# Kernel tuning notes

Hardware: AMD Instinct MI355X
Metric: run time of the kernel (lower is better)

## Reference

```python
import jax, jax.numpy as jnp
import numpy as np

H = 256  # n_hidden


def _lstm_layer(x, W_ih, W_hh, b):
    # x: [B, T, D]; W_ih: [4H, D]; W_hh: [4H, H]; b: [4H]
    B = x.shape[0]
    xg = jnp.einsum('btd,gd->btg', x, W_ih) + b  # [B, T, 4H] input projection, precomputed
    xg = jnp.swapaxes(xg, 0, 1)  # [T, B, 4H] for scan over time

    def step(carry, xt):
        h, c = carry
        g = xt + h @ W_hh.T  # [B, 4H]
        i = jax.nn.sigmoid(g[:, 0 * H:1 * H])
        f = jax.nn.sigmoid(g[:, 1 * H:2 * H])
        gg = jnp.tanh(g[:, 2 * H:3 * H])
        o = jax.nn.sigmoid(g[:, 3 * H:4 * H])
        c = f * c + i * gg
        h = o * jnp.tanh(c)
        return (h, c), h

    init = (jnp.zeros((B, H), x.dtype), jnp.zeros((B, H), x.dtype))
    (_, _), hs = jax.lax.scan(step, init, xg)
    return jnp.swapaxes(hs, 0, 1)  # [B, T, H]


def setup_inputs() -> dict:
    key = jax.random.key(0)
    ks = jax.random.split(key, 9)
    B, T, D, C = 256, 1024, 128, 10
    s_in, s_h = 1.0 / np.sqrt(D), 1.0 / np.sqrt(H)
    return {
        'x': jax.random.normal(ks[0], (B, T, D), jnp.float32),
        'W_ih0': jax.random.normal(ks[1], (4 * H, D), jnp.float32) * s_in,
        'W_hh0': jax.random.normal(ks[2], (4 * H, H), jnp.float32) * s_h,
        'b0': jax.random.normal(ks[3], (4 * H,), jnp.float32) * s_h,
        'W_ih1': jax.random.normal(ks[4], (4 * H, H), jnp.float32) * s_h,
        'W_hh1': jax.random.normal(ks[5], (4 * H, H), jnp.float32) * s_h,
        'b1': jax.random.normal(ks[6], (4 * H,), jnp.float32) * s_h,
        'Wd': jax.random.normal(ks[7], (C, H), jnp.float32) * s_h,
        'bd': jax.random.normal(ks[8], (C,), jnp.float32) * 0.01,
    }


def reference(x, W_ih0, W_hh0, b0, W_ih1, W_hh1, b1, Wd, bd):
    o = _lstm_layer(x, W_ih0, W_hh0, b0)   # layer 1
    o = _lstm_layer(o, W_ih1, W_hh1, b1)   # layer 2
    last = o[:, -1]                         # [B, H] last timestep
    logits = last @ Wd.T + bd               # [B, C]
    return jax.nn.softmax(logits, axis=1)
```

## Files before the change

### kernel.cpp

```cpp
#include <hip/hip_runtime.h>

#define TT 1024

typedef _Float16 f16;
typedef _Float16 f16x8 __attribute__((ext_vector_type(8)));
typedef float f32x4 __attribute__((ext_vector_type(4)));
typedef unsigned long long u64;

__device__ __forceinline__ float sigmoidf_(float x) { return 1.0f / (1.0f + __expf(-x)); }
__device__ __forceinline__ float tanhf_(float x) { return 1.0f - 2.0f / (__expf(2.0f * x) + 1.0f); }

__device__ __forceinline__ f16x8 load_frag_agent(const f16* p) {
  union { u64 v[2]; f16x8 f; } u;
  u.v[0] = __hip_atomic_load((u64*)p,     __ATOMIC_RELAXED, __HIP_MEMORY_SCOPE_AGENT);
  u.v[1] = __hip_atomic_load((u64*)p + 1, __ATOMIC_RELAXED, __HIP_MEMORY_SCOPE_AGENT);
  return u.f;
}

__device__ __forceinline__ void load_h8_sc0(const f16* p, f16x8* a) {
  asm volatile(
      "global_load_dwordx4 %0, %8, off sc0\n\t"
      "global_load_dwordx4 %1, %8, off offset:64 sc0\n\t"
      "global_load_dwordx4 %2, %8, off offset:128 sc0\n\t"
      "global_load_dwordx4 %3, %8, off offset:192 sc0\n\t"
      "global_load_dwordx4 %4, %8, off offset:256 sc0\n\t"
      "global_load_dwordx4 %5, %8, off offset:320 sc0\n\t"
      "global_load_dwordx4 %6, %8, off offset:384 sc0\n\t"
      "global_load_dwordx4 %7, %8, off offset:448 sc0\n\t"
      "s_waitcnt vmcnt(0)"
      : "=&v"(a[0]), "=&v"(a[1]), "=&v"(a[2]), "=&v"(a[3]),
        "=&v"(a[4]), "=&v"(a[5]), "=&v"(a[6]), "=&v"(a[7])
      : "v"(p)
      : "memory");
}
__device__ __forceinline__ void load_h16_sc0(const f16* p0, const f16* p1, f16x8* a) {
  asm volatile(
      "global_load_dwordx4 %0, %16, off sc0\n\t"
      "global_load_dwordx4 %1, %16, off offset:64 sc0\n\t"
      "global_load_dwordx4 %2, %16, off offset:128 sc0\n\t"
      "global_load_dwordx4 %3, %16, off offset:192 sc0\n\t"
      "global_load_dwordx4 %4, %16, off offset:256 sc0\n\t"
      "global_load_dwordx4 %5, %16, off offset:320 sc0\n\t"
      "global_load_dwordx4 %6, %16, off offset:384 sc0\n\t"
      "global_load_dwordx4 %7, %16, off offset:448 sc0\n\t"
      "global_load_dwordx4 %8, %17, off sc0\n\t"
      "global_load_dwordx4 %9, %17, off offset:64 sc0\n\t"
      "global_load_dwordx4 %10, %17, off offset:128 sc0\n\t"
      "global_load_dwordx4 %11, %17, off offset:192 sc0\n\t"
      "global_load_dwordx4 %12, %17, off offset:256 sc0\n\t"
      "global_load_dwordx4 %13, %17, off offset:320 sc0\n\t"
      "global_load_dwordx4 %14, %17, off offset:384 sc0\n\t"
      "global_load_dwordx4 %15, %17, off offset:448 sc0\n\t"
      "s_waitcnt vmcnt(0)"
      : "=&v"(a[0]), "=&v"(a[1]), "=&v"(a[2]), "=&v"(a[3]),
        "=&v"(a[4]), "=&v"(a[5]), "=&v"(a[6]), "=&v"(a[7]),
        "=&v"(a[8]), "=&v"(a[9]), "=&v"(a[10]), "=&v"(a[11]),
        "=&v"(a[12]), "=&v"(a[13]), "=&v"(a[14]), "=&v"(a[15])
      : "v"(p0), "v"(p1)
      : "memory");
}

template <int LAYER>
__device__ __forceinline__ void group_barrier(unsigned* slots, int role, unsigned e, int tid) {
  __syncthreads();
  __atomic_signal_fence(__ATOMIC_SEQ_CST);
  if (tid == 0)
    __hip_atomic_store(slots + role * 64, e, __ATOMIC_RELAXED, __HIP_MEMORY_SCOPE_AGENT);
  if (tid < 64) {
    const int s = tid & 31;
    const unsigned thr = (LAYER == 0 && s >= 16) ? e - 1u : e;
    for (;;) {
      unsigned v = __hip_atomic_load(slots + s * 64, __ATOMIC_RELAXED,
                                     __HIP_MEMORY_SCOPE_AGENT);
      if (__all(v >= thr)) break;
      __builtin_amdgcn_s_sleep(2);
    }
  }
  __atomic_signal_fence(__ATOMIC_SEQ_CST);
  __syncthreads();
}

template <int LAYER, bool LOCAL>
__device__ void run_layer(const float* __restrict__ xin, const f16* __restrict__ in2base,
                          const float* __restrict__ Wih, const float* __restrict__ Whh,
                          const float* __restrict__ bias, f16* __restrict__ hself,
                          unsigned* slots, int role, int ng, int b0r,
                          float (*Gs)[68], int tid) {
  constexpr int NCH = (LAYER == 0) ? 12 : 16;
  constexpr int DIN = (LAYER == 0) ? 128 : 256;

  const int lane = tid & 63, wave = tid >> 6;
  const int q = lane >> 4, mm = lane & 15;
  const int rw = wave & 1, uw = wave >> 1;
  const int u0 = ng * 16 + uw * 8;

  const int up_e = tid & 7, bl_e = tid >> 3;
  const int uwe = up_e >> 2, ppe = up_e & 3;
  const int uc0 = ng * 16 + uwe * 8 + 2 * ppe, uc1 = uc0 + 1;
  const int gcol = uwe * 32 + 2 * ppe;
  const float bi0 = bias[uc0],       bi1 = bias[uc1];
  const float bf0 = bias[256 + uc0], bf1 = bias[256 + uc1];
  const float bg0 = bias[512 + uc0], bg1 = bias[512 + uc1];
  const float bo0 = bias[768 + uc0], bo1 = bias[768 + uc1];

  const int row0 = ((mm >> 3)) * 256 + u0 + (mm & 7);
  const int row1 = ((mm >> 3) + 2) * 256 + u0 + (mm & 7);
  f16x8 bA[NCH], bB[NCH];
#pragma unroll
  for (int c = 0; c < NCH; ++c) {
    const int k0 = c * 32 + q * 8;
    const float* s0 = (c < 8) ? (Whh + row0 * 256 + k0) : (Wih + row0 * DIN + (k0 - 256));
    const float* s1 = (c < 8) ? (Whh + row1 * 256 + k0) : (Wih + row1 * DIN + (k0 - 256));
    f16x8 v0, v1;
#pragma unroll
    for (int j = 0; j < 8; ++j) { v0[j] = (f16)s0[j]; v1[j] = (f16)s1[j]; }
    bA[c] = v0; bB[c] = v1;
  }

  float cA = 0.f, cB = 0.f;
  const int brow = b0r + rw * 16 + mm;

  float4 axr[8];
  f16x8 ax[4];

  for (int it = 0; it <= TT + 1; ++it) {
    const int i = it - 1;
    const bool active = (LAYER == 0) ? (i >= 0 && i < TT) : (i >= 1 && i <= TT);

    if (LAYER == 0 && active) {
#pragma unroll
      for (int c = 0; c < 4; ++c) {
        const float4 fa = axr[2 * c], fb = axr[2 * c + 1];
        f16x8 v; v[0]=(f16)fa.x; v[1]=(f16)fa.y; v[2]=(f16)fa.z; v[3]=(f16)fa.w;
        v[4]=(f16)fb.x; v[5]=(f16)fb.y; v[6]=(f16)fb.z; v[7]=(f16)fb.w;
        ax[c] = v;
      }
    }

    f16x8 a[NCH];
    if (active) {
      const f16* hprev = (LAYER == 0) ? (hself + ((i + 2) % 3) * 65536)
                                      : (hself + ((i + 1) & 1) * 65536);
      const f16* pa1 = hprev + brow * 256 + q * 8;
      if (LAYER == 0) {
        if constexpr (LOCAL) load_h8_sc0(pa1, a);
        else {
#pragma unroll
          for (int c = 0; c < 8; ++c) a[c] = load_frag_agent(pa1 + c * 32);
        }
#pragma unroll
        for (int c = 8; c < NCH; ++c) a[c] = ax[c - 8];
      } else {
        const f16* pa2 = in2base + ((i + 2) % 3) * 65536 + brow * 256 + q * 8;
        if constexpr (LOCAL) load_h16_sc0(pa1, pa2, a);
        else {
#pragma unroll
          for (int c = 0; c < 8; ++c) a[c] = load_frag_agent(pa1 + c * 32);
#pragma unroll
          for (int c = 8; c < NCH; ++c) a[c] = load_frag_agent(pa2 + (c - 8) * 32);
        }
      }
    }

    if (LAYER == 0 && it < TT) {
      const float* px = xin + (brow * 1024 + it) * 128 + q * 8;
#pragma unroll
      for (int c = 0; c < 4; ++c) {
        axr[2 * c]     = *(const float4*)(px + c * 32);
        axr[2 * c + 1] = *(const float4*)(px + c * 32 + 4);
      }
    }

    if (active) {
      f32x4 acc0 = {0.f, 0.f, 0.f, 0.f}, acc1 = {0.f, 0.f, 0.f, 0.f};
#pragma unroll
      for (int c = 0; c < NCH; ++c) {
        acc0 = __builtin_amdgcn_mfma_f32_16x16x32_f16(a[c], bA[c], acc0, 0, 0, 0);
        acc1 = __builtin_amdgcn_mfma_f32_16x16x32_f16(a[c], bB[c], acc1, 0, 0, 0);
      }
#pragma unroll
      for (int r = 0; r < 4; ++r) {
        Gs[rw * 16 + q * 4 + r][uw * 32 + mm] = acc0[r];
        Gs[rw * 16 + q * 4 + r][uw * 32 + 16 + mm] = acc1[r];
      }
      __syncthreads();
      {
        f16* hout = (LAYER == 0) ? (hself + (i % 3) * 65536)
                                 : (hself + (i & 1) * 65536);
        const float gi0 = Gs[bl_e][gcol]      + bi0, gi1 = Gs[bl_e][gcol + 1]  + bi1;
        const float gf0 = Gs[bl_e][gcol + 8]  + bf0, gf1 = Gs[bl_e][gcol + 9]  + bf1;
        const float gg0 = Gs[bl_e][gcol + 16] + bg0, gg1 = Gs[bl_e][gcol + 17] + bg1;
        const float go0 = Gs[bl_e][gcol + 24] + bo0, go1 = Gs[bl_e][gcol + 25] + bo1;
        cA = sigmoidf_(gf0) * cA + sigmoidf_(gi0) * tanhf_(gg0);
        cB = sigmoidf_(gf1) * cB + sigmoidf_(gi1) * tanhf_(gg1);
        union { f16 h2v[2]; unsigned u; } pk;
        pk.h2v[0] = (f16)(sigmoidf_(go0) * tanhf_(cA));
        pk.h2v[1] = (f16)(sigmoidf_(go1) * tanhf_(cB));
        unsigned* dst = (unsigned*)(hout + (b0r + bl_e) * 256 + uc0);
        if constexpr (LOCAL) {
          *dst = pk.u;
        } else {
          __hip_atomic_store(dst, pk.u, __ATOMIC_RELAXED, __HIP_MEMORY_SCOPE_AGENT);
        }
      }
    }

    if (it <= TT) group_barrier<LAYER>(slots, role, (unsigned)(it + 1), tid);
  }
}

__global__ __launch_bounds__(256, 1) void lstm_persistent(
    const float* __restrict__ x,
    const float* __restrict__ Wih0, const float* __restrict__ Whh0, const float* __restrict__ b0v,
    const float* __restrict__ Wih1, const float* __restrict__ Whh1, const float* __restrict__ b1v,
    f16* h1buf, f16* h2buf, unsigned* F) {
  __shared__ float Gs[32][68];
  __shared__ int sh[3];
  const int tid = threadIdx.x;

  if (tid == 0) {
    unsigned xcc = __builtin_amdgcn_s_getreg(63508) & 7u;
    unsigned* NG = F + 32;
    unsigned rank = __hip_atomic_fetch_add(&NG[xcc], 1u, __ATOMIC_RELAXED, __HIP_MEMORY_SCOPE_AGENT);
    __hip_atomic_fetch_add(&NG[8], 1u, __ATOMIC_RELEASE, __HIP_MEMORY_SCOPE_AGENT);
    while (__hip_atomic_load(&NG[8], __ATOMIC_ACQUIRE, __HIP_MEMORY_SCOPE_AGENT) < 256u)
      __builtin_amdgcn_s_sleep(8);
    unsigned cnt[8];
#pragma unroll
    for (int xx = 0; xx < 8; ++xx)
      cnt[xx] = __hip_atomic_load(&NG[xx], __ATOMIC_RELAXED, __HIP_MEMORY_SCOPE_AGENT);
    int group, role2;
    if (rank < 32u) {
      group = (int)xcc; role2 = (int)rank;
    } else {
      int ov = (int)rank - 32;
      for (int xx = 0; xx < (int)xcc; ++xx) ov += max(0, (int)cnt[xx] - 32);
      int gg = 0, acc = 0;
      for (gg = 0; gg < 8; ++gg) {
        const int d = 32 - min(32, (int)cnt[gg]);
        if (ov < acc + d) break;
        acc += d;
      }
      if (gg > 7) gg = 7;
      group = gg; role2 = min(31, (int)cnt[gg] + (ov - acc));
    }
    sh[0] = group; sh[1] = role2; sh[2] = (cnt[group] >= 32u) ? 1 : 0;
  }
  __syncthreads();
  const int group = sh[0], role = sh[1], local = sh[2];
  unsigned* slots = F + group * 2048;
  const int b0r = group * 32;
  const int layer = role >> 4, ng = role & 15;

  if (layer == 0) {
    if (local) run_layer<0, true >(x, nullptr, Wih0, Whh0, b0v, h1buf, slots, role, ng, b0r, Gs, tid);
    else       run_layer<0, false>(x, nullptr, Wih0, Whh0, b0v, h1buf, slots, role, ng, b0r, Gs, tid);
  } else {
    if (local) run_layer<1, true >(nullptr, h1buf, Wih1, Whh1, b1v, h2buf, slots, role, ng, b0r, Gs, tid);
    else       run_layer<1, false>(nullptr, h1buf, Wih1, Whh1, b1v, h2buf, slots, role, ng, b0r, Gs, tid);
  }
}

__global__ __launch_bounds__(64, 1) void dense_softmax_k(const f16* __restrict__ h2,
                                                         const float* __restrict__ Wd,
                                                         const float* __restrict__ bd,
                                                         float* __restrict__ out) {
  const int b = blockIdx.x, lane = threadIdx.x;
  float hv[4];
#pragma unroll
  for (int j = 0; j < 4; ++j) hv[j] = (float)h2[b * 256 + lane + 64 * j];
  float p[10];
#pragma unroll
  for (int c = 0; c < 10; ++c) {
    float s = 0.f;
#pragma unroll
    for (int j = 0; j < 4; ++j) s += hv[j] * Wd[c * 256 + lane + 64 * j];
#pragma unroll
    for (int off = 32; off >= 1; off >>= 1) s += __shfl_xor(s, off, 64);
    p[c] = s;
  }
  if (lane == 0) {
    float mx = -1e30f;
#pragma unroll
    for (int c = 0; c < 10; ++c) { p[c] += bd[c]; mx = fmaxf(mx, p[c]); }
    float den = 0.f;
#pragma unroll
    for (int c = 0; c < 10; ++c) { p[c] = __expf(p[c] - mx); den += p[c]; }
#pragma unroll
    for (int c = 0; c < 10; ++c) out[b * 10 + c] = p[c] / den;
  }
}

extern "C" void kernel_launch(void* const* d_in, const int* in_sizes, int n_in,
                              void* d_out, int out_size, void* d_ws, size_t ws_size,
                              hipStream_t stream) {
  const float* x    = (const float*)d_in[0];
  const float* Wih0 = (const float*)d_in[1];
  const float* Whh0 = (const float*)d_in[2];
  const float* b0v  = (const float*)d_in[3];
  const float* Wih1 = (const float*)d_in[4];
  const float* Whh1 = (const float*)d_in[5];
  const float* b1v  = (const float*)d_in[6];
  const float* Wd   = (const float*)d_in[7];
  const float* bd   = (const float*)d_in[8];

  char* ws = (char*)d_ws;
  f16* h1buf = (f16*)(ws);
  f16* h2buf = (f16*)(ws + 384 * 1024);
  unsigned* F = (unsigned*)(ws + 640 * 1024);

  hipMemsetAsync(ws + 256 * 1024, 0, 256 * 1024, stream);
  hipMemsetAsync(ws + 640 * 1024, 0, 64 * 1024, stream);

  lstm_persistent<<<256, 256, 0, stream>>>(x, Wih0, Whh0, b0v, Wih1, Whh1, b1v,
                                           h1buf, h2buf, F);
  dense_softmax_k<<<256, 64, 0, stream>>>(h2buf, Wd, bd, (float*)d_out);
}
```

Before: 3.714 ms.

## Use per-wave LDS gate exchange and raw barriers to shorten the recurrent step

Each wave now stages its own MFMA gate tile in a private LDS slice and computes the LSTM cell update for the rows and units it produced. This removes the block-wide __syncthreads between the matmul and the elementwise phase. The x prefetch for the next timestep is moved after the h store. The group barrier now uses raw s_barrier with a partial vmcnt wait, so the in-flight x loads are not drained before synchronisation. The risk is subtle memory-ordering bugs with the hand-written waitcnt, plus a changed cell-state ownership mapping that must match the earlier layout.

```diff
diff --git a/kernel.cpp b/kernel.cpp
--- a/kernel.cpp
+++ b/kernel.cpp
@@ -60,32 +60,12 @@
       : "memory");
 }
 
-template <int LAYER>
-__device__ __forceinline__ void group_barrier(unsigned* slots, int role, unsigned e, int tid) {
-  __syncthreads();
-  __atomic_signal_fence(__ATOMIC_SEQ_CST);
-  if (tid == 0)
-    __hip_atomic_store(slots + role * 64, e, __ATOMIC_RELAXED, __HIP_MEMORY_SCOPE_AGENT);
-  if (tid < 64) {
-    const int s = tid & 31;
-    const unsigned thr = (LAYER == 0 && s >= 16) ? e - 1u : e;
-    for (;;) {
-      unsigned v = __hip_atomic_load(slots + s * 64, __ATOMIC_RELAXED,
-                                     __HIP_MEMORY_SCOPE_AGENT);
-      if (__all(v >= thr)) break;
-      __builtin_amdgcn_s_sleep(2);
-    }
-  }
-  __atomic_signal_fence(__ATOMIC_SEQ_CST);
-  __syncthreads();
-}
-
 template <int LAYER, bool LOCAL>
 __device__ void run_layer(const float* __restrict__ xin, const f16* __restrict__ in2base,
                           const float* __restrict__ Wih, const float* __restrict__ Whh,
                           const float* __restrict__ bias, f16* __restrict__ hself,
                           unsigned* slots, int role, int ng, int b0r,
-                          float (*Gs)[68], int tid) {
+                          float* GsBase, int tid) {
   constexpr int NCH = (LAYER == 0) ? 12 : 16;
   constexpr int DIN = (LAYER == 0) ? 128 : 256;
 
@@ -93,11 +73,11 @@
   const int q = lane >> 4, mm = lane & 15;
   const int rw = wave & 1, uw = wave >> 1;
   const int u0 = ng * 16 + uw * 8;
-
-  const int up_e = tid & 7, bl_e = tid >> 3;
-  const int uwe = up_e >> 2, ppe = up_e & 3;
-  const int uc0 = ng * 16 + uwe * 8 + 2 * ppe, uc1 = uc0 + 1;
-  const int gcol = uwe * 32 + 2 * ppe;
+  float* Gw = GsBase + wave * 544;
+
+  const int re = lane >> 2, pe = lane & 3;
+  const int uc0 = ng * 16 + uw * 8 + 2 * pe, uc1 = uc0 + 1;
+  const int erow = b0r + rw * 16 + re;
   const float bi0 = bias[uc0],       bi1 = bias[uc1];
   const float bf0 = bias[256 + uc0], bf1 = bias[256 + uc1];
   const float bg0 = bias[512 + uc0], bg1 = bias[512 + uc1];
@@ -137,11 +117,11 @@
       }
     }
 
-    f16x8 a[NCH];
     if (active) {
       const f16* hprev = (LAYER == 0) ? (hself + ((i + 2) % 3) * 65536)
                                       : (hself + ((i + 1) & 1) * 65536);
       const f16* pa1 = hprev + brow * 256 + q * 8;
+      f16x8 a[NCH];
       if (LAYER == 0) {
         if constexpr (LOCAL) load_h8_sc0(pa1, a);
         else {
@@ -160,8 +140,45 @@
           for (int c = 8; c < NCH; ++c) a[c] = load_frag_agent(pa2 + (c - 8) * 32);
         }
       }
-    }
-
+
+      f32x4 acc0 = {0.f, 0.f, 0.f, 0.f}, acc1 = {0.f, 0.f, 0.f, 0.f};
+#pragma unroll
+      for (int c = 0; c < NCH; ++c) {
+        acc0 = __builtin_amdgcn_mfma_f32_16x16x32_f16(a[c], bA[c], acc0, 0, 0, 0);
+        acc1 = __builtin_amdgcn_mfma_f32_16x16x32_f16(a[c], bB[c], acc1, 0, 0, 0);
+      }
+
+#pragma unroll
+      for (int r = 0; r < 4; ++r) {
+        Gw[(q * 4 + r) * 34 + mm]      = acc0[r];
+        Gw[(q * 4 + r) * 34 + 16 + mm] = acc1[r];
+      }
+      asm volatile("" ::: "memory");
+      const float2 vi = *(const float2*)(Gw + re * 34 + 2 * pe);
+      const float2 vf = *(const float2*)(Gw + re * 34 + 8 + 2 * pe);
+      const float2 vg = *(const float2*)(Gw + re * 34 + 16 + 2 * pe);
+      const float2 vo = *(const float2*)(Gw + re * 34 + 24 + 2 * pe);
+
+      f16* hout = (LAYER == 0) ? (hself + (i % 3) * 65536)
+                               : (hself + (i & 1) * 65536);
+      const float gi0 = vi.x + bi0, gi1 = vi.y + bi1;
+      const float gf0 = vf.x + bf0, gf1 = vf.y + bf1;
+      const float gg0 = vg.x + bg0, gg1 = vg.y + bg1;
+      const float go0 = vo.x + bo0, go1 = vo.y + bo1;
+      cA = sigmoidf_(gf0) * cA + sigmoidf_(gi0) * tanhf_(gg0);
+      cB = sigmoidf_(gf1) * cB + sigmoidf_(gi1) * tanhf_(gg1);
+      union { f16 h2v[2]; unsigned u; } pk;
+      pk.h2v[0] = (f16)(sigmoidf_(go0) * tanhf_(cA));
+      pk.h2v[1] = (f16)(sigmoidf_(go1) * tanhf_(cB));
+      unsigned* dst = (unsigned*)(hout + erow * 256 + uc0);
+      if constexpr (LOCAL) {
+        *dst = pk.u;
+      } else {
+        __hip_atomic_store(dst, pk.u, __ATOMIC_RELAXED, __HIP_MEMORY_SCOPE_AGENT);
+      }
+    }
+
+    asm volatile("" ::: "memory");
     if (LAYER == 0 && it < TT) {
       const float* px = xin + (brow * 1024 + it) * 128 + q * 8;
 #pragma unroll
@@ -171,41 +188,31 @@
       }
     }
 
-    if (active) {
-      f32x4 acc0 = {0.f, 0.f, 0.f, 0.f}, acc1 = {0.f, 0.f, 0.f, 0.f};
-#pragma unroll
-      for (int c = 0; c < NCH; ++c) {
-        acc0 = __builtin_amdgcn_mfma_f32_16x16x32_f16(a[c], bA[c], acc0, 0, 0, 0);
-        acc1 = __builtin_amdgcn_mfma_f32_16x16x32_f16(a[c], bB[c], acc1, 0, 0, 0);
-      }
-#pragma unroll
-      for (int r = 0; r < 4; ++r) {
-        Gs[rw * 16 + q * 4 + r][uw * 32 + mm] = acc0[r];
-        Gs[rw * 16 + q * 4 + r][uw * 32 + 16 + mm] = acc1[r];
-      }
-      __syncthreads();
-      {
-        f16* hout = (LAYER == 0) ? (hself + (i % 3) * 65536)
-                                 : (hself + (i & 1) * 65536);
-        const float gi0 = Gs[bl_e][gcol]      + bi0, gi1 = Gs[bl_e][gcol + 1]  + bi1;
-        const float gf0 = Gs[bl_e][gcol + 8]  + bf0, gf1 = Gs[bl_e][gcol + 9]  + bf1;
-        const float gg0 = Gs[bl_e][gcol + 16] + bg0, gg1 = Gs[bl_e][gcol + 17] + bg1;
-        const float go0 = Gs[bl_e][gcol + 24] + bo0, go1 = Gs[bl_e][gcol + 25] + bo1;
-        cA = sigmoidf_(gf0) * cA + sigmoidf_(gi0) * tanhf_(gg0);
-        cB = sigmoidf_(gf1) * cB + sigmoidf_(gi1) * tanhf_(gg1);
-        union { f16 h2v[2]; unsigned u; } pk;
-        pk.h2v[0] = (f16)(sigmoidf_(go0) * tanhf_(cA));
-        pk.h2v[1] = (f16)(sigmoidf_(go1) * tanhf_(cB));
-        unsigned* dst = (unsigned*)(hout + (b0r + bl_e) * 256 + uc0);
-        if constexpr (LOCAL) {
-          *dst = pk.u;
-        } else {
-          __hip_atomic_store(dst, pk.u, __ATOMIC_RELAXED, __HIP_MEMORY_SCOPE_AGENT);
+    if (it <= TT) {
+      if (LAYER == 0 && it < TT) {
+        asm volatile("s_waitcnt vmcnt(8)" ::: "memory");
+      } else {
+        asm volatile("s_waitcnt vmcnt(0)" ::: "memory");
+      }
+      __builtin_amdgcn_s_barrier();
+      __atomic_signal_fence(__ATOMIC_SEQ_CST);
+      if (tid == 0)
+        __hip_atomic_store(slots + role * 64, (unsigned)(it + 1), __ATOMIC_RELAXED,
+                           __HIP_MEMORY_SCOPE_AGENT);
+      if (tid < 64) {
+        const int s = tid & 31;
+        const unsigned e = (unsigned)(it + 1);
+        const unsigned thr = (LAYER == 0 && s >= 16) ? e - 1u : e;
+        for (;;) {
+          unsigned v = __hip_atomic_load(slots + s * 64, __ATOMIC_RELAXED,
+                                         __HIP_MEMORY_SCOPE_AGENT);
+          if (__all(v >= thr)) break;
+          __builtin_amdgcn_s_sleep(2);
         }
       }
-    }
-
-    if (it <= TT) group_barrier<LAYER>(slots, role, (unsigned)(it + 1), tid);
+      __atomic_signal_fence(__ATOMIC_SEQ_CST);
+      __builtin_amdgcn_s_barrier();
+    }
   }
 }
 
@@ -214,7 +221,7 @@
     const float* __restrict__ Wih0, const float* __restrict__ Whh0, const float* __restrict__ b0v,
     const float* __restrict__ Wih1, const float* __restrict__ Whh1, const float* __restrict__ b1v,
     f16* h1buf, f16* h2buf, unsigned* F) {
-  __shared__ float Gs[32][68];
+  __shared__ float Gs[4 * 544];
   __shared__ int sh[3];
   const int tid = threadIdx.x;
 
```

After: 3.785 ms. About the same (+1.9%).

## Halve LSTM persistent grid by giving each block 32 hidden units

Applied to the files above, without the earlier changes.

Each block now owns 32 hidden units instead of 16, holding two sets of weight fragments in registers and issuing twice the MFMAs per step. The grid shrinks from 256 to 128 blocks, with 16 blocks per batch group, so each group barrier polls half as many slots. The gate epilogue handles four units per thread with float4 shared-memory reads and a 64-bit h store. This cuts cross-block synchronisation and communication per timestep, at the cost of doubled per-block compute and register pressure, which may cause spills.

```diff
diff --git a/kernel.cpp b/kernel.cpp
--- a/kernel.cpp
+++ b/kernel.cpp
@@ -67,8 +67,8 @@
   if (tid == 0)
     __hip_atomic_store(slots + role * 64, e, __ATOMIC_RELAXED, __HIP_MEMORY_SCOPE_AGENT);
   if (tid < 64) {
-    const int s = tid & 31;
-    const unsigned thr = (LAYER == 0 && s >= 16) ? e - 1u : e;
+    const int s = tid & 15;
+    const unsigned thr = (LAYER == 0 && s >= 8) ? e - 1u : e;
     for (;;) {
       unsigned v = __hip_atomic_load(slots + s * 64, __ATOMIC_RELAXED,
                                      __HIP_MEMORY_SCOPE_AGENT);
@@ -85,39 +85,42 @@
                           const float* __restrict__ Wih, const float* __restrict__ Whh,
                           const float* __restrict__ bias, f16* __restrict__ hself,
                           unsigned* slots, int role, int ng, int b0r,
-                          float (*Gs)[68], int tid) {
+                          float (*Gs)[132], int tid) {
   constexpr int NCH = (LAYER == 0) ? 12 : 16;
   constexpr int DIN = (LAYER == 0) ? 128 : 256;
 
   const int lane = tid & 63, wave = tid >> 6;
   const int q = lane >> 4, mm = lane & 15;
   const int rw = wave & 1, uw = wave >> 1;
-  const int u0 = ng * 16 + uw * 8;
-
-  const int up_e = tid & 7, bl_e = tid >> 3;
-  const int uwe = up_e >> 2, ppe = up_e & 3;
-  const int uc0 = ng * 16 + uwe * 8 + 2 * ppe, uc1 = uc0 + 1;
-  const int gcol = uwe * 32 + 2 * ppe;
-  const float bi0 = bias[uc0],       bi1 = bias[uc1];
-  const float bf0 = bias[256 + uc0], bf1 = bias[256 + uc1];
-  const float bg0 = bias[512 + uc0], bg1 = bias[512 + uc1];
-  const float bo0 = bias[768 + uc0], bo1 = bias[768 + uc1];
-
-  const int row0 = ((mm >> 3)) * 256 + u0 + (mm & 7);
-  const int row1 = ((mm >> 3) + 2) * 256 + u0 + (mm & 7);
-  f16x8 bA[NCH], bB[NCH];
-#pragma unroll
-  for (int c = 0; c < NCH; ++c) {
-    const int k0 = c * 32 + q * 8;
-    const float* s0 = (c < 8) ? (Whh + row0 * 256 + k0) : (Wih + row0 * DIN + (k0 - 256));
-    const float* s1 = (c < 8) ? (Whh + row1 * 256 + k0) : (Wih + row1 * DIN + (k0 - 256));
-    f16x8 v0, v1;
-#pragma unroll
-    for (int j = 0; j < 8; ++j) { v0[j] = (f16)s0[j]; v1[j] = (f16)s1[j]; }
-    bA[c] = v0; bB[c] = v1;
-  }
-
-  float cA = 0.f, cB = 0.f;
+
+  const int er = tid >> 3, up = tid & 7;
+  const int ubl = 4 * up;
+  const int uc0 = ng * 32 + ubl;
+  const int pcol = (ubl >> 3) * 32 + (ubl & 7);
+  const float4 bi4 = *(const float4*)(bias + uc0);
+  const float4 bf4 = *(const float4*)(bias + 256 + uc0);
+  const float4 bg4 = *(const float4*)(bias + 512 + uc0);
+  const float4 bo4 = *(const float4*)(bias + 768 + uc0);
+
+  f16x8 bA[2][NCH], bB[2][NCH];
+#pragma unroll
+  for (int sub = 0; sub < 2; ++sub) {
+    const int u0s = ng * 32 + uw * 16 + sub * 8;
+    const int row0 = ((mm >> 3)) * 256 + u0s + (mm & 7);
+    const int row1 = ((mm >> 3) + 2) * 256 + u0s + (mm & 7);
+#pragma unroll
+    for (int c = 0; c < NCH; ++c) {
+      const int k0 = c * 32 + q * 8;
+      const float* s0 = (c < 8) ? (Whh + row0 * 256 + k0) : (Wih + row0 * DIN + (k0 - 256));
+      const float* s1 = (c < 8) ? (Whh + row1 * 256 + k0) : (Wih + row1 * DIN + (k0 - 256));
+      f16x8 v0, v1;
+#pragma unroll
+      for (int j = 0; j < 8; ++j) { v0[j] = (f16)s0[j]; v1[j] = (f16)s1[j]; }
+      bA[sub][c] = v0; bB[sub][c] = v1;
+    }
+  }
+
+  float c0 = 0.f, c1 = 0.f, c2 = 0.f, c3 = 0.f;
   const int brow = b0r + rw * 16 + mm;
 
   float4 axr[8];
@@ -172,31 +175,47 @@
     }
 
     if (active) {
-      f32x4 acc0 = {0.f, 0.f, 0.f, 0.f}, acc1 = {0.f, 0.f, 0.f, 0.f};
+      f32x4 ac[2][2];
+#pragma unroll
+      for (int sub = 0; sub < 2; ++sub) {
+        ac[sub][0] = (f32x4){0.f, 0.f, 0.f, 0.f};
+        ac[sub][1] = (f32x4){0.f, 0.f, 0.f, 0.f};
+      }
 #pragma unroll
       for (int c = 0; c < NCH; ++c) {
-        acc0 = __builtin_amdgcn_mfma_f32_16x16x32_f16(a[c], bA[c], acc0, 0, 0, 0);
-        acc1 = __builtin_amdgcn_mfma_f32_16x16x32_f16(a[c], bB[c], acc1, 0, 0, 0);
-      }
-#pragma unroll
-      for (int r = 0; r < 4; ++r) {
-        Gs[rw * 16 + q * 4 + r][uw * 32 + mm] = acc0[r];
-        Gs[rw * 16 + q * 4 + r][uw * 32 + 16 + mm] = acc1[r];
+#pragma unroll
+        for (int sub = 0; sub < 2; ++sub) {
+          ac[sub][0] = __builtin_amdgcn_mfma_f32_16x16x32_f16(a[c], bA[sub][c], ac[sub][0], 0, 0, 0);
+          ac[sub][1] = __builtin_amdgcn_mfma_f32_16x16x32_f16(a[c], bB[sub][c], ac[sub][1], 0, 0, 0);
+        }
+      }
+#pragma unroll
+      for (int sub = 0; sub < 2; ++sub) {
+        const int p = uw * 2 + sub;
+#pragma unroll
+        for (int r = 0; r < 4; ++r) {
+          Gs[rw * 16 + q * 4 + r][p * 32 + mm]      = ac[sub][0][r];
+          Gs[rw * 16 + q * 4 + r][p * 32 + 16 + mm] = ac[sub][1][r];
+        }
       }
       __syncthreads();
       {
         f16* hout = (LAYER == 0) ? (hself + (i % 3) * 65536)
                                  : (hself + (i & 1) * 65536);
-        const float gi0 = Gs[bl_e][gcol]      + bi0, gi1 = Gs[bl_e][gcol + 1]  + bi1;
-        const float gf0 = Gs[bl_e][gcol + 8]  + bf0, gf1 = Gs[bl_e][gcol + 9]  + bf1;
-        const float gg0 = Gs[bl_e][gcol + 16] + bg0, gg1 = Gs[bl_e][gcol + 17] + bg1;
-        const float go0 = Gs[bl_e][gcol + 24] + bo0, go1 = Gs[bl_e][gcol + 25] + bo1;
-        cA = sigmoidf_(gf0) * cA + sigmoidf_(gi0) * tanhf_(gg0);
-        cB = sigmoidf_(gf1) * cB + sigmoidf_(gi1) * tanhf_(gg1);
-        union { f16 h2v[2]; unsigned u; } pk;
-        pk.h2v[0] = (f16)(sigmoidf_(go0) * tanhf_(cA));
-        pk.h2v[1] = (f16)(sigmoidf_(go1) * tanhf_(cB));
-        unsigned* dst = (unsigned*)(hout + (b0r + bl_e) * 256 + uc0);
+        const float4 gi = *(const float4*)&Gs[er][pcol];
+        const float4 gf = *(const float4*)&Gs[er][pcol + 8];
+        const float4 gg = *(const float4*)&Gs[er][pcol + 16];
+        const float4 go = *(const float4*)&Gs[er][pcol + 24];
+        c0 = sigmoidf_(gf.x + bf4.x) * c0 + sigmoidf_(gi.x + bi4.x) * tanhf_(gg.x + bg4.x);
+        c1 = sigmoidf_(gf.y + bf4.y) * c1 + sigmoidf_(gi.y + bi4.y) * tanhf_(gg.y + bg4.y);
+        c2 = sigmoidf_(gf.z + bf4.z) * c2 + sigmoidf_(gi.z + bi4.z) * tanhf_(gg.z + bg4.z);
+        c3 = sigmoidf_(gf.w + bf4.w) * c3 + sigmoidf_(gi.w + bi4.w) * tanhf_(gg.w + bg4.w);
+        union { f16 h4[4]; u64 u; } pk;
+        pk.h4[0] = (f16)(sigmoidf_(go.x + bo4.x) * tanhf_(c0));
+        pk.h4[1] = (f16)(sigmoidf_(go.y + bo4.y) * tanhf_(c1));
+        pk.h4[2] = (f16)(sigmoidf_(go.z + bo4.z) * tanhf_(c2));
+        pk.h4[3] = (f16)(sigmoidf_(go.w + bo4.w) * tanhf_(c3));
+        u64* dst = (u64*)(hout + (b0r + er) * 256 + uc0);
         if constexpr (LOCAL) {
           *dst = pk.u;
         } else {
@@ -214,7 +233,7 @@
     const float* __restrict__ Wih0, const float* __restrict__ Whh0, const float* __restrict__ b0v,
     const float* __restrict__ Wih1, const float* __restrict__ Whh1, const float* __restrict__ b1v,
     f16* h1buf, f16* h2buf, unsigned* F) {
-  __shared__ float Gs[32][68];
+  __shared__ float Gs[32][132];
   __shared__ int sh[3];
   const int tid = threadIdx.x;
 
@@ -223,34 +242,34 @@
     unsigned* NG = F + 32;
     unsigned rank = __hip_atomic_fetch_add(&NG[xcc], 1u, __ATOMIC_RELAXED, __HIP_MEMORY_SCOPE_AGENT);
     __hip_atomic_fetch_add(&NG[8], 1u, __ATOMIC_RELEASE, __HIP_MEMORY_SCOPE_AGENT);
-    while (__hip_atomic_load(&NG[8], __ATOMIC_ACQUIRE, __HIP_MEMORY_SCOPE_AGENT) < 256u)
+    while (__hip_atomic_load(&NG[8], __ATOMIC_ACQUIRE, __HIP_MEMORY_SCOPE_AGENT) < 128u)
       __builtin_amdgcn_s_sleep(8);
     unsigned cnt[8];
 #pragma unroll
     for (int xx = 0; xx < 8; ++xx)
       cnt[xx] = __hip_atomic_load(&NG[xx], __ATOMIC_RELAXED, __HIP_MEMORY_SCOPE_AGENT);
     int group, role2;
-    if (rank < 32u) {
+    if (rank < 16u) {
       group = (int)xcc; role2 = (int)rank;
     } else {
-      int ov = (int)rank - 32;
-      for (int xx = 0; xx < (int)xcc; ++xx) ov += max(0, (int)cnt[xx] - 32);
+      int ov = (int)rank - 16;
+      for (int xx = 0; xx < (int)xcc; ++xx) ov += max(0, (int)cnt[xx] - 16);
       int gg = 0, acc = 0;
       for (gg = 0; gg < 8; ++gg) {
-        const int d = 32 - min(32, (int)cnt[gg]);
+        const int d = 16 - min(16, (int)cnt[gg]);
         if (ov < acc + d) break;
         acc += d;
       }
       if (gg > 7) gg = 7;
-      group = gg; role2 = min(31, (int)cnt[gg] + (ov - acc));
-    }
-    sh[0] = group; sh[1] = role2; sh[2] = (cnt[group] >= 32u) ? 1 : 0;
+      group = gg; role2 = min(15, (int)cnt[gg] + (ov - acc));
+    }
+    sh[0] = group; sh[1] = role2; sh[2] = (cnt[group] >= 16u) ? 1 : 0;
   }
   __syncthreads();
   const int group = sh[0], role = sh[1], local = sh[2];
   unsigned* slots = F + group * 2048;
   const int b0r = group * 32;
-  const int layer = role >> 4, ng = role & 15;
+  const int layer = role >> 3, ng = role & 7;
 
   if (layer == 0) {
     if (local) run_layer<0, true >(x, nullptr, Wih0, Whh0, b0v, h1buf, slots, role, ng, b0r, Gs, tid);
@@ -312,7 +331,7 @@
   hipMemsetAsync(ws + 256 * 1024, 0, 256 * 1024, stream);
   hipMemsetAsync(ws + 640 * 1024, 0, 64 * 1024, stream);
 
-  lstm_persistent<<<256, 256, 0, stream>>>(x, Wih0, Whh0, b0v, Wih1, Whh1, b1v,
+  lstm_persistent<<<128, 256, 0, stream>>>(x, Wih0, Whh0, b0v, Wih1, Whh1, b1v,
                                            h1buf, h2buf, F);
   dense_softmax_k<<<256, 64, 0, stream>>>(h2buf, Wd, bd, (float*)d_out);
 }
```

Result: slower. 4.163 ms (+12.1%).
